# Optimization experiments

Hardware: AMD Instinct MI355X
Metric: run time of the kernel (lower is better)

The kernel has to match this reference:

```python
import jax, jax.numpy as jnp
import numpy as np

B, L, D, H = 4, 2048, 1024, 16
DH = D // H
SCALE = 1.0 / float(np.sqrt(DH))


def setup_inputs() -> dict:
    key = jax.random.key(0)
    ks = jax.random.split(key, 11)
    s = 0.02
    return {
        "q": jax.random.normal(ks[0], (B, L, D), jnp.float32),
        "k": jax.random.normal(ks[1], (B, L, D), jnp.float32),
        "v": jax.random.normal(ks[2], (B, L, D), jnp.float32),
        "Wq": jax.random.normal(ks[3], (D, D), jnp.float32) * s,
        "bq": jnp.zeros((D,), jnp.float32),
        "Wk": jax.random.normal(ks[4], (D, D), jnp.float32) * s,
        "bk": jnp.zeros((D,), jnp.float32),
        "Wv": jax.random.normal(ks[5], (D, D), jnp.float32) * s,
        "bv": jnp.zeros((D,), jnp.float32),
        "Wo": jax.random.normal(ks[6], (D, D), jnp.float32) * s,
        "bo": jnp.zeros((D,), jnp.float32),
    }


def _split_heads(x):
    # (B, L, D) -> (B, H, L, DH)
    b, l, _ = x.shape
    return x.reshape(b, l, H, DH).transpose(0, 2, 1, 3)


def reference(q, k, v, Wq, bq, Wk, bk, Wv, bv, Wo, bo):
    # torch Linear: y = x @ W.T + b
    qh = _split_heads(q @ Wq.T + bq)
    kh = _split_heads(k @ Wk.T + bk)
    vh = _split_heads(v @ Wv.T + bv)
    # Blocked loop in original == full attention: every q block sees all K/V.
    scores = jnp.einsum("bhqd,bhkd->bhqk", qh, kh) * SCALE
    attn = jax.nn.softmax(scores, axis=-1)  # dropout=0 (eval) -> identity
    out = jnp.einsum("bhqk,bhkd->bhqd", attn, vh)
    out = out.transpose(0, 2, 1, 3).reshape(q.shape[0], q.shape[1], D)
    return out @ Wo.T + bo
```

## Files before the change

kernel.cpp:

```cpp
#include <hip/hip_runtime.h>
#include <hip/hip_bf16.h>
#include <stdint.h>

#define NB  4
#define SEQ 2048
#define DIM 1024
#define NH  16
#define DHD 64
#define LOG2E 1.44269504088896340736f

typedef short short8 __attribute__((ext_vector_type(8)));
typedef float f32x4  __attribute__((ext_vector_type(4)));

__device__ __forceinline__ unsigned short f2bf(float f) {
  union { float f; uint32_t u; } x; x.f = f;
  uint32_t u = x.u;
  uint32_t r = (u + 0x7fffu + ((u >> 16) & 1u)) >> 16;
  return (unsigned short)r;
}

__device__ __forceinline__ uint32_t cvt_pk_bf16(float lo, float hi) {
  uint32_t r;
  asm("v_cvt_pk_bf16_f32 %0, %1, %2" : "=v"(r) : "v"(lo), "v"(hi));
  return r;
}

__device__ __forceinline__ void gload16(const void* g, void* l) {
  __builtin_amdgcn_global_load_lds(
      (const __attribute__((address_space(1))) uint32_t*)g,
      (__attribute__((address_space(3))) uint32_t*)l, 16, 0, 0);
}

__global__ void cvt_f32_bf16(const float* __restrict__ in,
                             unsigned short* __restrict__ out, int n4) {
  int i = blockIdx.x * blockDim.x + threadIdx.x;
  int stride = gridDim.x * blockDim.x;
  for (int j = i; j < n4; j += stride) {
    float4 v = reinterpret_cast<const float4*>(in)[j];
    ushort4 o;
    o.x = f2bf(v.x); o.y = f2bf(v.y); o.z = f2bf(v.z); o.w = f2bf(v.w);
    reinterpret_cast<ushort4*>(out)[j] = o;
  }
}

template <int MODE>
__global__ __launch_bounds__(256, 2) void gemm_bt(
    const unsigned short* __restrict__ A,
    const unsigned short* __restrict__ Bm,
    const float* __restrict__ bias,
    float* __restrict__ Cf,
    unsigned short* __restrict__ Cb,
    int M, int N, int K, float scale) {
  __shared__ uint4 smem[4096];

  const int tid  = threadIdx.x;
  const int lane = tid & 63;
  const int wid  = tid >> 6;
  const int cpx  = gridDim.x >> 3;
  const int wg   = (blockIdx.x & 7) * cpx + (blockIdx.x >> 3);
  const int nbn  = N >> 7;
  const int bm   = wg / nbn;
  const int bn   = wg % nbn;
  const int wrow = (wid >> 1) * 64;
  const int wcol = (wid & 1) * 64;

  f32x4 acc[4][4] = {};

  const unsigned short* pa[4];
  const unsigned short* pb[4];
  uint4* la[4];
  uint4* lb[4];
#pragma unroll
  for (int i = 0; i < 4; ++i) {
    int c   = tid + (i << 8);
    int row = c >> 3;
    int kc  = (c & 7) ^ (row & 7);
    pa[i] = A  + (size_t)(bm * 128 + row) * K + kc * 8;
    pb[i] = Bm + (size_t)(bn * 128 + row) * K + kc * 8;
    la[i] = smem + c;
    lb[i] = smem + 2048 + c;
  }
  auto stage = [&](int kt, int buf) {
#pragma unroll
    for (int i = 0; i < 4; ++i) {
      gload16(pa[i] + kt * 64, la[i] + buf * 1024);
      gload16(pb[i] + kt * 64, lb[i] + buf * 1024);
    }
  };

  stage(0, 0);
  __syncthreads();

  const int NT = K >> 6;
  for (int kt = 0; kt < NT; ++kt) {
    const int cur = kt & 1;
    if (kt + 1 < NT) stage(kt + 1, cur ^ 1);

#pragma unroll
    for (int s = 0; s < 2; ++s) {
      short8 af[4], bfr[4];
#pragma unroll
      for (int mt = 0; mt < 4; ++mt) {
        int row = wrow + mt * 16 + (lane & 15);
        int ch  = ((s << 2) + (lane >> 4)) ^ (row & 7);
        af[mt]  = __builtin_bit_cast(short8, smem[cur * 1024 + row * 8 + ch]);
      }
#pragma unroll
      for (int nt = 0; nt < 4; ++nt) {
        int row = wcol + nt * 16 + (lane & 15);
        int ch  = ((s << 2) + (lane >> 4)) ^ (row & 7);
        bfr[nt] = __builtin_bit_cast(short8, smem[2048 + cur * 1024 + row * 8 + ch]);
      }
      __builtin_amdgcn_s_setprio(1);
#pragma unroll
      for (int mt = 0; mt < 4; ++mt)
#pragma unroll
        for (int nt = 0; nt < 4; ++nt)
          acc[mt][nt] = __builtin_amdgcn_mfma_f32_16x16x32_bf16(af[mt], bfr[nt], acc[mt][nt], 0, 0, 0);
      __builtin_amdgcn_s_setprio(0);
    }
    __syncthreads();
  }

  if (MODE == 0) {
    float* cf = (float*)smem;
#pragma unroll
    for (int nt = 0; nt < 4; ++nt) {
      int tcol = wcol + nt * 16 + (lane & 15);
      float bv = bias[bn * 128 + tcol];
#pragma unroll
      for (int mt = 0; mt < 4; ++mt)
#pragma unroll
        for (int r = 0; r < 4; ++r) {
          int trow = wrow + mt * 16 + (lane >> 4) * 4 + r;
          cf[trow * 128 + tcol] = acc[mt][nt][r] + bv;
        }
    }
    __syncthreads();
#pragma unroll
    for (int it = 0; it < 16; ++it) {
      int idx = tid + it * 256;
      int row = idx >> 5, seg = idx & 31;
      uint4 val = ((uint4*)cf)[idx];
      *reinterpret_cast<uint4*>(Cf + (size_t)(bm * 128 + row) * N + bn * 128 + seg * 4) = val;
    }
  } else if (MODE == 1) {
    unsigned short* cb = (unsigned short*)smem;
#pragma unroll
    for (int nt = 0; nt < 4; ++nt) {
      int tcol = wcol + nt * 16 + (lane & 15);
      float bv = bias[bn * 128 + tcol];
#pragma unroll
      for (int mt = 0; mt < 4; ++mt)
#pragma unroll
        for (int r = 0; r < 4; ++r) {
          int trow = wrow + mt * 16 + (lane >> 4) * 4 + r;
          cb[trow * 128 + tcol] = f2bf((acc[mt][nt][r] + bv) * scale);
        }
    }
    __syncthreads();
#pragma unroll
    for (int it = 0; it < 8; ++it) {
      int idx = tid + it * 256;
      int row = idx >> 4, seg = idx & 15;
      uint4 val = ((uint4*)cb)[idx];
      int gcol = bn * 128 + seg * 8;
      int h = gcol >> 6, dh = gcol & 63;
      int grow = bm * 128 + row;
      int b = grow >> 11, lq = grow & 2047;
      *reinterpret_cast<uint4*>(Cb + ((size_t)((b << 4) + h) * SEQ + lq) * DHD + dh) = val;
    }
  } else {
    unsigned short* cb = (unsigned short*)smem;
#pragma unroll
    for (int nt = 0; nt < 4; ++nt) {
      int tcol = wcol + nt * 16 + (lane & 15);
      float bv = bias[bn * 128 + tcol];
#pragma unroll
      for (int mt = 0; mt < 4; ++mt) {
        int trow0 = wrow + mt * 16 + (lane >> 4) * 4;
        uint2 pk;
        pk.x = cvt_pk_bf16((acc[mt][nt][0] + bv) * scale, (acc[mt][nt][1] + bv) * scale);
        pk.y = cvt_pk_bf16((acc[mt][nt][2] + bv) * scale, (acc[mt][nt][3] + bv) * scale);
        *reinterpret_cast<uint2*>(cb + tcol * 128 + trow0) = pk;
      }
    }
    __syncthreads();
#pragma unroll
    for (int it = 0; it < 8; ++it) {
      int idx = tid + it * 256;
      int col = idx >> 4, seg = idx & 15;
      uint4 val = ((uint4*)cb)[idx];
      int gcol = bn * 128 + col;
      int h = gcol >> 6, dh = gcol & 63;
      int grow = bm * 128 + seg * 8;
      int b = grow >> 11, lq = grow & 2047;
      *reinterpret_cast<uint4*>(Cb + ((size_t)((b << 4) + h) * DHD + dh) * SEQ + lq) = val;
    }
  }
}

__global__ __launch_bounds__(512, 4) void attn_kernel(
    const unsigned short* __restrict__ Qh,
    const unsigned short* __restrict__ Kh,
    const unsigned short* __restrict__ Vt,
    unsigned short* __restrict__ O) {
  __shared__ uint4 Kls[2][512];
  __shared__ uint4 Vls[2][512];
  __shared__ uint4 Pls[8][32 * 9];

  const int tid  = threadIdx.x;
  const int lane = tid & 63;
  const int wid  = tid >> 6;
  const int wg   = (blockIdx.x & 7) * 64 + (blockIdx.x >> 3);
  const int bh   = wg >> 3;
  const int qt   = wg & 7;
  const int qloc = lane & 15;
  const int grp  = lane >> 4;
  const int q7   = qloc & 7;

  const unsigned short* Qb = Qh + (size_t)bh * SEQ * DHD;
  const unsigned short* Kb = Kh + (size_t)bh * SEQ * DHD;
  const unsigned short* Vb = Vt + (size_t)bh * DHD * SEQ;

  const int srow = tid >> 3;
  const int skc  = (tid & 7) ^ (srow & 7);
  const unsigned short* pk0 = Kb + (size_t)srow * DHD + skc * 8;
  const unsigned short* pv0 = Vb + (size_t)srow * SEQ + skc * 8;
  auto stage = [&](int kt, int buf) {
    gload16(pk0 + (size_t)kt * 64 * DHD, &Kls[buf][tid]);
    gload16(pv0 + kt * 64,               &Vls[buf][tid]);
  };

  stage(0, 0);

  short8 qf[2][2];
#pragma unroll
  for (int qb = 0; qb < 2; ++qb) {
    int qrow = qt * 256 + wid * 32 + qb * 16 + qloc;
#pragma unroll
    for (int s = 0; s < 2; ++s)
      qf[qb][s] = *reinterpret_cast<const short8*>(Qb + (size_t)qrow * DHD + s * 32 + grp * 8);
  }

  const short8 ones = {0x3F80, 0x3F80, 0x3F80, 0x3F80, 0x3F80, 0x3F80, 0x3F80, 0x3F80};
  char* pwb = (char*)&Pls[wid][0];

  __syncthreads();

  float logbias = 0.f;
  f32x4 lsum[2] = {};
  f32x4 acc_o[4][2] = {};

  const int NT = SEQ / 64;
  for (int kt = 0; kt < NT; ++kt) {
    const int cur = kt & 1;
    if (kt + 1 < NT) stage(kt + 1, cur ^ 1);

    f32x4 sc[4][2];
    __builtin_amdgcn_s_setprio(1);
#pragma unroll
    for (int j = 0; j < 4; ++j) {
      short8 kf[2];
#pragma unroll
      for (int s = 0; s < 2; ++s) {
        int krow = j * 16 + qloc;
        int ch   = ((s << 2) + grp) ^ q7;
        kf[s] = __builtin_bit_cast(short8, Kls[cur][krow * 8 + ch]);
      }
#pragma unroll
      for (int qb = 0; qb < 2; ++qb) {
        f32x4 a = {logbias, logbias, logbias, logbias};
        a = __builtin_amdgcn_mfma_f32_16x16x32_bf16(kf[0], qf[qb][0], a, 0, 0, 0);
        a = __builtin_amdgcn_mfma_f32_16x16x32_bf16(kf[1], qf[qb][1], a, 0, 0, 0);
        sc[j][qb] = a;
      }
    }
    __builtin_amdgcn_s_setprio(0);

#pragma unroll
    for (int j = 0; j < 4; ++j)
#pragma unroll
      for (int qb = 0; qb < 2; ++qb) {
        float p0 = exp2f(sc[j][qb][0]);
        float p1 = exp2f(sc[j][qb][1]);
        float p2 = exp2f(sc[j][qb][2]);
        float p3 = exp2f(sc[j][qb][3]);
        uint2 w;
        w.x = cvt_pk_bf16(p0, p1);
        w.y = cvt_pk_bf16(p2, p3);
        *(uint2*)(pwb + (qb * 16 + qloc) * 144 + j * 32 + grp * 8) = w;
      }

    short8 pf[2][2];
#pragma unroll
    for (int qb = 0; qb < 2; ++qb)
#pragma unroll
      for (int t = 0; t < 2; ++t)
        pf[qb][t] = *(const short8*)(pwb + (qb * 16 + qloc) * 144 + t * 64 + grp * 16);

    __builtin_amdgcn_s_setprio(1);
#pragma unroll
    for (int db = 0; db < 4; ++db) {
      short8 vf[2];
#pragma unroll
      for (int t = 0; t < 2; ++t) {
        int vrow = db * 16 + qloc;
        int ch   = ((t << 2) + grp) ^ q7;
        vf[t] = __builtin_bit_cast(short8, Vls[cur][vrow * 8 + ch]);
      }
#pragma unroll
      for (int qb = 0; qb < 2; ++qb) {
        acc_o[db][qb] = __builtin_amdgcn_mfma_f32_16x16x32_bf16(vf[0], pf[qb][0], acc_o[db][qb], 0, 0, 0);
        acc_o[db][qb] = __builtin_amdgcn_mfma_f32_16x16x32_bf16(vf[1], pf[qb][1], acc_o[db][qb], 0, 0, 0);
      }
    }
#pragma unroll
    for (int qb = 0; qb < 2; ++qb) {
      lsum[qb] = __builtin_amdgcn_mfma_f32_16x16x32_bf16(ones, pf[qb][0], lsum[qb], 0, 0, 0);
      lsum[qb] = __builtin_amdgcn_mfma_f32_16x16x32_bf16(ones, pf[qb][1], lsum[qb], 0, 0, 0);
    }
    __builtin_amdgcn_s_setprio(0);

    if (__any(fmaxf(lsum[0][0], lsum[1][0]) > 7.9e28f)) {
      const float ds = 5.421010862e-20f;
      logbias -= 64.f;
#pragma unroll
      for (int db = 0; db < 4; ++db)
#pragma unroll
        for (int qb = 0; qb < 2; ++qb)
#pragma unroll
          for (int r = 0; r < 4; ++r) acc_o[db][qb][r] *= ds;
#pragma unroll
      for (int qb = 0; qb < 2; ++qb)
#pragma unroll
        for (int r = 0; r < 4; ++r) lsum[qb][r] *= ds;
    }

    __syncthreads();
  }

  const float inv0 = 1.0f / lsum[0][0];
  const float inv1 = 1.0f / lsum[1][0];
#pragma unroll
  for (int db = 0; db < 4; ++db)
#pragma unroll
    for (int qb = 0; qb < 2; ++qb) {
      float inv = qb ? inv1 : inv0;
      uint2 w;
      w.x = cvt_pk_bf16(acc_o[db][qb][0] * inv, acc_o[db][qb][1] * inv);
      w.y = cvt_pk_bf16(acc_o[db][qb][2] * inv, acc_o[db][qb][3] * inv);
      *(uint2*)(pwb + (qb * 16 + qloc) * 144 + db * 32 + grp * 8) = w;
    }
  const int b = bh >> 4, h = bh & 15;
#pragma unroll
  for (int pass = 0; pass < 4; ++pass) {
    int idx = pass * 64 + lane;
    int row = idx >> 3;
    int ck  = idx & 7;
    uint4 val = *(const uint4*)(pwb + row * 144 + ck * 16);
    int rowg = qt * 256 + wid * 32 + row;
    *reinterpret_cast<uint4*>(O + ((size_t)(b * SEQ + rowg)) * DIM + (h << 6) + ck * 8) = val;
  }
}

extern "C" void kernel_launch(void* const* d_in, const int* in_sizes, int n_in,
                              void* d_out, int out_size, void* d_ws, size_t ws_size,
                              hipStream_t stream) {
  (void)in_sizes; (void)n_in; (void)out_size; (void)ws_size;
  const float* q  = (const float*)d_in[0];
  const float* k  = (const float*)d_in[1];
  const float* v  = (const float*)d_in[2];
  const float* Wq = (const float*)d_in[3];
  const float* bq = (const float*)d_in[4];
  const float* Wk = (const float*)d_in[5];
  const float* bk = (const float*)d_in[6];
  const float* Wv = (const float*)d_in[7];
  const float* bv = (const float*)d_in[8];
  const float* Wo = (const float*)d_in[9];
  const float* bo = (const float*)d_in[10];
  float* out = (float*)d_out;

  char* ws = (char*)d_ws;
  const size_t MB = 1024 * 1024;
  unsigned short* X   = (unsigned short*)(ws + 0);
  unsigned short* WX  = (unsigned short*)(ws + 16 * MB);
  unsigned short* Qhp = (unsigned short*)(ws + 18 * MB);
  unsigned short* Khp = (unsigned short*)(ws + 34 * MB);
  unsigned short* Vtp = (unsigned short*)(ws + 50 * MB);

  const int nTok = NB * SEQ * DIM;
  const int nW   = DIM * DIM;
  const int M    = NB * SEQ;
  dim3 gg((M / 128) * (DIM / 128));

  cvt_f32_bf16<<<2048, 256, 0, stream>>>(q, X, nTok / 4);
  cvt_f32_bf16<<<1024, 256, 0, stream>>>(Wq, WX, nW / 4);
  gemm_bt<1><<<gg, 256, 0, stream>>>(X, WX, bq, nullptr, Qhp, M, DIM, DIM, 0.125f * LOG2E);
  cvt_f32_bf16<<<2048, 256, 0, stream>>>(k, X, nTok / 4);
  cvt_f32_bf16<<<1024, 256, 0, stream>>>(Wk, WX, nW / 4);
  gemm_bt<1><<<gg, 256, 0, stream>>>(X, WX, bk, nullptr, Khp, M, DIM, DIM, 1.0f);
  cvt_f32_bf16<<<2048, 256, 0, stream>>>(v, X, nTok / 4);
  cvt_f32_bf16<<<1024, 256, 0, stream>>>(Wv, WX, nW / 4);
  gemm_bt<2><<<gg, 256, 0, stream>>>(X, WX, bv, nullptr, Vtp, M, DIM, DIM, 1.0f);
  attn_kernel<<<NB * NH * (SEQ / 256), 512, 0, stream>>>(Qhp, Khp, Vtp, X);
  cvt_f32_bf16<<<1024, 256, 0, stream>>>(Wo, WX, nW / 4);
  gemm_bt<0><<<gg, 256, 0, stream>>>(X, WX, bo, out, nullptr, M, DIM, DIM, 1.0f);
}
```

Before: 233.5 us.

## Fuse fp32-to-bf16 activation conversion into GEMM A-tile staging and batch weight casts

The projection GEMMs now read fp32 activations directly through registers, convert them to bf16 with packed converts and write them into LDS after the MFMA loop. This removes the separate activation conversion kernels and their round trip through global memory. The four weight conversions are merged into one launch when the workspace is large enough. The epilogues now write straight to global memory instead of staging through LDS, which risks less coalesced stores, and the register-staged A path replaces asynchronous global-to-LDS loads for A.

After: 210.8 us. -9.7%, faster.

```diff
diff --git a/kernel.cpp b/kernel.cpp
--- a/kernel.cpp
+++ b/kernel.cpp
@@ -43,9 +43,27 @@
   }
 }
 
-template <int MODE>
+__global__ void cvt_w4(const float* __restrict__ w0, const float* __restrict__ w1,
+                       const float* __restrict__ w2, const float* __restrict__ w3,
+                       unsigned short* __restrict__ o0, unsigned short* __restrict__ o1,
+                       unsigned short* __restrict__ o2, unsigned short* __restrict__ o3,
+                       int n4) {
+  int seg = blockIdx.x >> 8;
+  int bid = blockIdx.x & 255;
+  const float* in = (seg == 0) ? w0 : (seg == 1) ? w1 : (seg == 2) ? w2 : w3;
+  unsigned short* out = (seg == 0) ? o0 : (seg == 1) ? o1 : (seg == 2) ? o2 : o3;
+  for (int j = bid * 256 + threadIdx.x; j < n4; j += 65536) {
+    float4 v = reinterpret_cast<const float4*>(in)[j];
+    ushort4 o;
+    o.x = f2bf(v.x); o.y = f2bf(v.y); o.z = f2bf(v.z); o.w = f2bf(v.w);
+    reinterpret_cast<ushort4*>(out)[j] = o;
+  }
+}
+
+template <int MODE, int AF32>
 __global__ __launch_bounds__(256, 2) void gemm_bt(
     const unsigned short* __restrict__ A,
+    const float* __restrict__ Af,
     const unsigned short* __restrict__ Bm,
     const float* __restrict__ bias,
     float* __restrict__ Cf,
@@ -67,6 +85,7 @@
   f32x4 acc[4][4] = {};
 
   const unsigned short* pa[4];
+  const float*          paf[4];
   const unsigned short* pb[4];
   uint4* la[4];
   uint4* lb[4];
@@ -75,26 +94,58 @@
     int c   = tid + (i << 8);
     int row = c >> 3;
     int kc  = (c & 7) ^ (row & 7);
-    pa[i] = A  + (size_t)(bm * 128 + row) * K + kc * 8;
-    pb[i] = Bm + (size_t)(bn * 128 + row) * K + kc * 8;
+    pa[i]  = A  + (size_t)(bm * 128 + row) * K + kc * 8;
+    paf[i] = Af + (size_t)(bm * 128 + row) * K + kc * 8;
+    pb[i]  = Bm + (size_t)(bn * 128 + row) * K + kc * 8;
     la[i] = smem + c;
     lb[i] = smem + 2048 + c;
   }
-  auto stage = [&](int kt, int buf) {
+
+  float4 a32[4][2];
+  auto loadA_f32 = [&](int kt) {
 #pragma unroll
     for (int i = 0; i < 4; ++i) {
-      gload16(pa[i] + kt * 64, la[i] + buf * 1024);
-      gload16(pb[i] + kt * 64, lb[i] + buf * 1024);
+      a32[i][0] = *reinterpret_cast<const float4*>(paf[i] + kt * 64);
+      a32[i][1] = *reinterpret_cast<const float4*>(paf[i] + kt * 64 + 4);
     }
   };
-
-  stage(0, 0);
+  auto writeA_bf16 = [&](int buf) {
+#pragma unroll
+    for (int i = 0; i < 4; ++i) {
+      uint4 w;
+      w.x = cvt_pk_bf16(a32[i][0].x, a32[i][0].y);
+      w.y = cvt_pk_bf16(a32[i][0].z, a32[i][0].w);
+      w.z = cvt_pk_bf16(a32[i][1].x, a32[i][1].y);
+      w.w = cvt_pk_bf16(a32[i][1].z, a32[i][1].w);
+      *(la[i] + buf * 1024) = w;
+    }
+  };
+  auto stageA_g = [&](int kt, int buf) {
+#pragma unroll
+    for (int i = 0; i < 4; ++i) gload16(pa[i] + kt * 64, la[i] + buf * 1024);
+  };
+  auto stageB = [&](int kt, int buf) {
+#pragma unroll
+    for (int i = 0; i < 4; ++i) gload16(pb[i] + kt * 64, lb[i] + buf * 1024);
+  };
+
+  if (AF32) {
+    loadA_f32(0);
+    writeA_bf16(0);
+  } else {
+    stageA_g(0, 0);
+  }
+  stageB(0, 0);
   __syncthreads();
 
   const int NT = K >> 6;
   for (int kt = 0; kt < NT; ++kt) {
     const int cur = kt & 1;
-    if (kt + 1 < NT) stage(kt + 1, cur ^ 1);
+    if (kt + 1 < NT) {
+      if (AF32) loadA_f32(kt + 1);
+      else      stageA_g(kt + 1, cur ^ 1);
+      stageB(kt + 1, cur ^ 1);
+    }
 
 #pragma unroll
     for (int s = 0; s < 2; ++s) {
@@ -119,83 +170,44 @@
           acc[mt][nt] = __builtin_amdgcn_mfma_f32_16x16x32_bf16(af[mt], bfr[nt], acc[mt][nt], 0, 0, 0);
       __builtin_amdgcn_s_setprio(0);
     }
+
+    if (AF32 && kt + 1 < NT) writeA_bf16(cur ^ 1);
     __syncthreads();
   }
 
-  if (MODE == 0) {
-    float* cf = (float*)smem;
-#pragma unroll
-    for (int nt = 0; nt < 4; ++nt) {
-      int tcol = wcol + nt * 16 + (lane & 15);
-      float bv = bias[bn * 128 + tcol];
-#pragma unroll
-      for (int mt = 0; mt < 4; ++mt)
-#pragma unroll
-        for (int r = 0; r < 4; ++r) {
-          int trow = wrow + mt * 16 + (lane >> 4) * 4 + r;
-          cf[trow * 128 + tcol] = acc[mt][nt][r] + bv;
-        }
-    }
-    __syncthreads();
-#pragma unroll
-    for (int it = 0; it < 16; ++it) {
-      int idx = tid + it * 256;
-      int row = idx >> 5, seg = idx & 31;
-      uint4 val = ((uint4*)cf)[idx];
-      *reinterpret_cast<uint4*>(Cf + (size_t)(bm * 128 + row) * N + bn * 128 + seg * 4) = val;
-    }
-  } else if (MODE == 1) {
-    unsigned short* cb = (unsigned short*)smem;
-#pragma unroll
-    for (int nt = 0; nt < 4; ++nt) {
-      int tcol = wcol + nt * 16 + (lane & 15);
-      float bv = bias[bn * 128 + tcol];
-#pragma unroll
-      for (int mt = 0; mt < 4; ++mt)
-#pragma unroll
-        for (int r = 0; r < 4; ++r) {
-          int trow = wrow + mt * 16 + (lane >> 4) * 4 + r;
-          cb[trow * 128 + tcol] = f2bf((acc[mt][nt][r] + bv) * scale);
-        }
-    }
-    __syncthreads();
-#pragma unroll
-    for (int it = 0; it < 8; ++it) {
-      int idx = tid + it * 256;
-      int row = idx >> 4, seg = idx & 15;
-      uint4 val = ((uint4*)cb)[idx];
-      int gcol = bn * 128 + seg * 8;
-      int h = gcol >> 6, dh = gcol & 63;
-      int grow = bm * 128 + row;
-      int b = grow >> 11, lq = grow & 2047;
-      *reinterpret_cast<uint4*>(Cb + ((size_t)((b << 4) + h) * SEQ + lq) * DHD + dh) = val;
-    }
-  } else {
-    unsigned short* cb = (unsigned short*)smem;
-#pragma unroll
-    for (int nt = 0; nt < 4; ++nt) {
-      int tcol = wcol + nt * 16 + (lane & 15);
-      float bv = bias[bn * 128 + tcol];
-#pragma unroll
-      for (int mt = 0; mt < 4; ++mt) {
-        int trow0 = wrow + mt * 16 + (lane >> 4) * 4;
+  const int rbase = bm * 128 + wrow + (lane >> 4) * 4;
+  const int cbase = bn * 128 + wcol + (lane & 15);
+#pragma unroll
+  for (int nt = 0; nt < 4; ++nt) {
+    int col  = cbase + nt * 16;
+    float bv = bias[col];
+#pragma unroll
+    for (int mt = 0; mt < 4; ++mt) {
+      if (MODE == 2) {
+        int h = col >> 6, dh = col & 63;
+        int row0 = rbase + mt * 16;
+        int b = row0 >> 11, lq = row0 & 2047;
         uint2 pk;
         pk.x = cvt_pk_bf16((acc[mt][nt][0] + bv) * scale, (acc[mt][nt][1] + bv) * scale);
         pk.y = cvt_pk_bf16((acc[mt][nt][2] + bv) * scale, (acc[mt][nt][3] + bv) * scale);
-        *reinterpret_cast<uint2*>(cb + tcol * 128 + trow0) = pk;
-      }
-    }
-    __syncthreads();
-#pragma unroll
-    for (int it = 0; it < 8; ++it) {
-      int idx = tid + it * 256;
-      int col = idx >> 4, seg = idx & 15;
-      uint4 val = ((uint4*)cb)[idx];
-      int gcol = bn * 128 + col;
-      int h = gcol >> 6, dh = gcol & 63;
-      int grow = bm * 128 + seg * 8;
-      int b = grow >> 11, lq = grow & 2047;
-      *reinterpret_cast<uint4*>(Cb + ((size_t)((b << 4) + h) * DHD + dh) * SEQ + lq) = val;
+        size_t dst = ((size_t)((b << 4) + h) * DHD + dh) * SEQ + lq;
+        *reinterpret_cast<uint2*>(Cb + dst) = pk;
+      } else {
+#pragma unroll
+        for (int r = 0; r < 4; ++r) {
+          int row = rbase + mt * 16 + r;
+          float v = acc[mt][nt][r] + bv;
+          if (MODE == 0) {
+            Cf[(size_t)row * N + col] = v;
+          } else {
+            v *= scale;
+            int h = col >> 6, dh = col & 63;
+            int b = row >> 11, lq = row & 2047;
+            size_t dst = ((size_t)((b << 4) + h) * SEQ + lq) * DHD + dh;
+            Cb[dst] = f2bf(v);
+          }
+        }
+      }
     }
   }
 }
@@ -359,7 +371,7 @@
     int row = idx >> 3;
     int ck  = idx & 7;
     uint4 val = *(const uint4*)(pwb + row * 144 + ck * 16);
-    int rowg = qt * 256 + wid * 32 + row;
+    int rowg  = qt * 256 + wid * 32 + row;
     *reinterpret_cast<uint4*>(O + ((size_t)(b * SEQ + rowg)) * DIM + (h << 6) + ck * 8) = val;
   }
 }
@@ -367,7 +379,7 @@
 extern "C" void kernel_launch(void* const* d_in, const int* in_sizes, int n_in,
                               void* d_out, int out_size, void* d_ws, size_t ws_size,
                               hipStream_t stream) {
-  (void)in_sizes; (void)n_in; (void)out_size; (void)ws_size;
+  (void)in_sizes; (void)n_in; (void)out_size;
   const float* q  = (const float*)d_in[0];
   const float* k  = (const float*)d_in[1];
   const float* v  = (const float*)d_in[2];
@@ -383,27 +395,42 @@
 
   char* ws = (char*)d_ws;
   const size_t MB = 1024 * 1024;
-  unsigned short* X   = (unsigned short*)(ws + 0);
-  unsigned short* WX  = (unsigned short*)(ws + 16 * MB);
-  unsigned short* Qhp = (unsigned short*)(ws + 18 * MB);
-  unsigned short* Khp = (unsigned short*)(ws + 34 * MB);
-  unsigned short* Vtp = (unsigned short*)(ws + 50 * MB);
-
-  const int nTok = NB * SEQ * DIM;
-  const int nW   = DIM * DIM;
-  const int M    = NB * SEQ;
+  const int nW = DIM * DIM;
+  const int M  = NB * SEQ;
   dim3 gg((M / 128) * (DIM / 128));
-
-  cvt_f32_bf16<<<2048, 256, 0, stream>>>(q, X, nTok / 4);
-  cvt_f32_bf16<<<1024, 256, 0, stream>>>(Wq, WX, nW / 4);
-  gemm_bt<1><<<gg, 256, 0, stream>>>(X, WX, bq, nullptr, Qhp, M, DIM, DIM, 0.125f * LOG2E);
-  cvt_f32_bf16<<<2048, 256, 0, stream>>>(k, X, nTok / 4);
-  cvt_f32_bf16<<<1024, 256, 0, stream>>>(Wk, WX, nW / 4);
-  gemm_bt<1><<<gg, 256, 0, stream>>>(X, WX, bk, nullptr, Khp, M, DIM, DIM, 1.0f);
-  cvt_f32_bf16<<<2048, 256, 0, stream>>>(v, X, nTok / 4);
-  cvt_f32_bf16<<<1024, 256, 0, stream>>>(Wv, WX, nW / 4);
-  gemm_bt<2><<<gg, 256, 0, stream>>>(X, WX, bv, nullptr, Vtp, M, DIM, DIM, 1.0f);
-  attn_kernel<<<NB * NH * (SEQ / 256), 512, 0, stream>>>(Qhp, Khp, Vtp, X);
-  cvt_f32_bf16<<<1024, 256, 0, stream>>>(Wo, WX, nW / 4);
-  gemm_bt<0><<<gg, 256, 0, stream>>>(X, WX, bo, out, nullptr, M, DIM, DIM, 1.0f);
-}
+  const int attnGrid = NB * NH * (SEQ / 256);
+
+  if (ws_size >= 73 * MB) {
+    unsigned short* X   = (unsigned short*)(ws + 0);
+    unsigned short* WXq = (unsigned short*)(ws + 16 * MB);
+    unsigned short* WXk = (unsigned short*)(ws + 18 * MB);
+    unsigned short* WXv = (unsigned short*)(ws + 20 * MB);
+    unsigned short* WXo = (unsigned short*)(ws + 22 * MB);
+    unsigned short* Qhp = (unsigned short*)(ws + 24 * MB);
+    unsigned short* Khp = (unsigned short*)(ws + 40 * MB);
+    unsigned short* Vtp = (unsigned short*)(ws + 56 * MB);
+
+    cvt_w4<<<1024, 256, 0, stream>>>(Wq, Wk, Wv, Wo, WXq, WXk, WXv, WXo, nW / 4);
+    gemm_bt<1, 1><<<gg, 256, 0, stream>>>(nullptr, q, WXq, bq, nullptr, Qhp, M, DIM, DIM, 0.125f * LOG2E);
+    gemm_bt<1, 1><<<gg, 256, 0, stream>>>(nullptr, k, WXk, bk, nullptr, Khp, M, DIM, DIM, 1.0f);
+    gemm_bt<2, 1><<<gg, 256, 0, stream>>>(nullptr, v, WXv, bv, nullptr, Vtp, M, DIM, DIM, 1.0f);
+    attn_kernel<<<attnGrid, 512, 0, stream>>>(Qhp, Khp, Vtp, X);
+    gemm_bt<0, 0><<<gg, 256, 0, stream>>>(X, nullptr, WXo, bo, out, nullptr, M, DIM, DIM, 1.0f);
+  } else {
+    unsigned short* X   = (unsigned short*)(ws + 0);
+    unsigned short* WX  = (unsigned short*)(ws + 16 * MB);
+    unsigned short* Qhp = (unsigned short*)(ws + 18 * MB);
+    unsigned short* Khp = (unsigned short*)(ws + 34 * MB);
+    unsigned short* Vtp = (unsigned short*)(ws + 50 * MB);
+
+    cvt_f32_bf16<<<1024, 256, 0, stream>>>(Wq, WX, nW / 4);
+    gemm_bt<1, 1><<<gg, 256, 0, stream>>>(nullptr, q, WX, bq, nullptr, Qhp, M, DIM, DIM, 0.125f * LOG2E);
+    cvt_f32_bf16<<<1024, 256, 0, stream>>>(Wk, WX, nW / 4);
+    gemm_bt<1, 1><<<gg, 256, 0, stream>>>(nullptr, k, WX, bk, nullptr, Khp, M, DIM, DIM, 1.0f);
+    cvt_f32_bf16<<<1024, 256, 0, stream>>>(Wv, WX, nW / 4);
+    gemm_bt<2, 1><<<gg, 256, 0, stream>>>(nullptr, v, WX, bv, nullptr, Vtp, M, DIM, DIM, 1.0f);
+    attn_kernel<<<attnGrid, 512, 0, stream>>>(Qhp, Khp, Vtp, X);
+    cvt_f32_bf16<<<1024, 256, 0, stream>>>(Wo, WX, nW / 4);
+    gemm_bt<0, 0><<<gg, 256, 0, stream>>>(X, nullptr, WX, bo, out, nullptr, M, DIM, DIM, 1.0f);
+  }
+}
```
